# Kernel optimization log

Measured on AMD Instinct MI355X. Metric: run time of the kernel, lower is better.

Reference implementation:

```python
import jax, jax.numpy as jnp
import numpy as np

B, S, D, K = 8, 4096, 256, 8192
BETA = 0.25


def setup_inputs() -> dict:
    key = jax.random.key(0)
    k1, k2 = jax.random.split(key)
    return {
        "z": jax.random.normal(k1, (B, S, D), dtype=jnp.float32),
        "embed": jax.random.normal(k2, (K, D), dtype=jnp.float32),
    }


def reference(z, embed):
    # Inference-path VQ-EMA forward (EMA buffer updates are a no-grad side
    # effect only active in training mode; excluded from the pure reference).
    num_codes, dim = embed.shape
    z_flat = z.reshape(-1, dim)                      # [N, D]
    # squared-euclidean distances: ||z||^2 - 2 z.e^T + ||e||^2  -> [N, K]
    dist = ((z_flat * z_flat).sum(1, keepdims=True)
            - 2.0 * (z_flat @ embed.T)
            + (embed * embed).sum(1)[None, :])
    idx = jnp.argmin(dist, axis=1)                   # [N]
    z_q = embed[idx].reshape(z.shape)                # gather instead of onehot @ embed
    # commitment loss: beta * mse(stop_grad(z_q), z)
    loss = BETA * jnp.mean(jnp.square(jax.lax.stop_gradient(z_q) - z))
    # straight-through estimator
    z_q_st = z + jax.lax.stop_gradient(z_q - z)
    # perplexity from code usage histogram (scatter-add instead of onehot.mean)
    counts = jnp.zeros((num_codes,), dtype=z.dtype).at[idx].add(1.0)
    avg_probs = counts / idx.shape[0]
    perplexity = jnp.exp(-jnp.sum(avg_probs * jnp.log(avg_probs + 1e-12)))
    return z_q_st, loss, perplexity, idx.reshape(z.shape[:-1])
```

## Files before the change

kernel.cpp:

```cpp
#include <hip/hip_runtime.h>
#include <stdint.h>
#include <math.h>

#define NROWS 32768
#define DIM   256
#define KCODES 8192
#define BETA  0.25f
#define RSPLIT 64
#define NELEM 8388608
#define TAU 0.09375f

typedef float f32x4 __attribute__((ext_vector_type(4)));
typedef _Float16 v8h __attribute__((ext_vector_type(8)));
typedef unsigned short us4 __attribute__((ext_vector_type(4)));

__device__ inline unsigned int split1(float x) {
    _Float16 hf = (_Float16)x;
    _Float16 lf = (_Float16)(x - (float)hf);
    unsigned int h = __builtin_bit_cast(unsigned short, hf);
    unsigned int l = __builtin_bit_cast(unsigned short, lf);
    return h | (l << 16);
}

__device__ inline void gload_lds16(const void* g, void* l) {
    __builtin_amdgcn_global_load_lds(
        (const __attribute__((address_space(1))) void*)g,
        (__attribute__((address_space(3))) void*)l,
        16, 0, 0);
}

__device__ inline unsigned int fkey(float f) {
    unsigned int b = __float_as_uint(f);
    return (b & 0x80000000u) ? ~b : (b | 0x80000000u);
}

__global__ void prep_all(const float* __restrict__ z,
                         const float* __restrict__ e,
                         unsigned short* __restrict__ zhi,
                         unsigned short* __restrict__ zlo,
                         unsigned short* __restrict__ ehi,
                         unsigned short* __restrict__ elo,
                         float* __restrict__ enrm,
                         float* __restrict__ counts,
                         float* __restrict__ lossAcc,
                         int* __restrict__ flagcnt) {
    if (blockIdx.x < 8192) {
        int t = blockIdx.x * 256 + threadIdx.x;
        float4 v = reinterpret_cast<const float4*>(z)[t];
        unsigned int p0 = split1(v.x);
        unsigned int p1 = split1(v.y);
        unsigned int p2 = split1(v.z);
        unsigned int p3 = split1(v.w);
        us4 h, l;
        h[0] = (unsigned short)p0; l[0] = (unsigned short)(p0 >> 16);
        h[1] = (unsigned short)p1; l[1] = (unsigned short)(p1 >> 16);
        h[2] = (unsigned short)p2; l[2] = (unsigned short)(p2 >> 16);
        h[3] = (unsigned short)p3; l[3] = (unsigned short)(p3 >> 16);
        reinterpret_cast<us4*>(zhi)[t] = h;
        reinterpret_cast<us4*>(zlo)[t] = l;
    } else {
        int row = blockIdx.x - 8192;
        int d = threadIdx.x;
        float x = e[(size_t)row * DIM + d];
        unsigned int p = split1(x);
        ehi[(size_t)row * DIM + d] = (unsigned short)p;
        elo[(size_t)row * DIM + d] = (unsigned short)(p >> 16);
        float sq = x * x;
        #pragma unroll
        for (int off = 32; off; off >>= 1) sq += __shfl_down(sq, off);
        __shared__ float ps[4];
        if ((threadIdx.x & 63) == 0) ps[threadIdx.x >> 6] = sq;
        __syncthreads();
        if (threadIdx.x == 0) {
            enrm[row] = 0.5f * (ps[0] + ps[1] + ps[2] + ps[3]);
            counts[row] = 0.f;
            if (row == 0) { *lossAcc = 0.f; *flagcnt = 0; }
        }
    }
}

__launch_bounds__(256, 2)
__global__ void gemm_hi_fused(const unsigned short* __restrict__ zhi,
                              const unsigned short* __restrict__ ehi,
                              const float* __restrict__ enrm,
                              int* __restrict__ colidx,
                              float* __restrict__ out_idx,
                              int* __restrict__ flagcnt,
                              int* __restrict__ flaglist,
                              unsigned long long* __restrict__ rkey) {
    __shared__ __align__(16) unsigned short Bs[4][128 * 64];
    __shared__ float rvv[4][64];
    __shared__ float rv2s[4][64];
    __shared__ int   rcc[4][64];

    const int tid = threadIdx.x;
    const int w = tid >> 6, l = tid & 63;
    const int lx = l & 15, quad = l >> 4;
    const int arow_base = blockIdx.x * 64;
    const int fr = lx & 7;
    const int ecol = w * 32 + lx;
    const int st_g = ((l & 7) ^ (l >> 3)) * 8;
    const int srow = tid >> 3;

    v8h af[4][8];
    #pragma unroll
    for (int mi = 0; mi < 4; ++mi) {
        const unsigned short* ap =
            zhi + (size_t)(arow_base + mi * 16 + lx) * DIM + quad * 8;
        #pragma unroll
        for (int ks = 0; ks < 8; ++ks)
            af[mi][ks] = *(const v8h*)(ap + ks * 32);
    }

    float esn0 = enrm[ecol];
    float esn1 = enrm[ecol + 16];

#define STAGE(BUF, NT, BK) do {                                               \
        const unsigned short* _s = ehi + (size_t)(NT) * (128 * DIM)           \
            + (size_t)srow * DIM + (BK) * 64 + st_g;                          \
        gload_lds16(_s,                    &Bs[BUF][(w * 8) * 64]);           \
        gload_lds16(_s + (size_t)32 * DIM, &Bs[BUF][(32 + w * 8) * 64]);      \
        gload_lds16(_s + (size_t)64 * DIM, &Bs[BUF][(64 + w * 8) * 64]);      \
        gload_lds16(_s + (size_t)96 * DIM, &Bs[BUF][(96 + w * 8) * 64]);      \
} while (0)

#define FENCE do {                                                            \
        asm volatile("s_waitcnt vmcnt(8)" ::: "memory");                      \
        __builtin_amdgcn_s_barrier();                                         \
        asm volatile("" ::: "memory");                                        \
} while (0)

#define READF(BUF) do {                                                       \
        _Pragma("unroll") for (int kc = 0; kc < 2; ++kc) {                    \
            const int gsw = ((kc * 4 + quad) ^ fr) * 8;                       \
            bf[kc * 2 + 0] = *(const v8h*)&Bs[BUF][(ecol) * 64 + gsw];        \
            bf[kc * 2 + 1] = *(const v8h*)&Bs[BUF][(ecol + 16) * 64 + gsw];   \
        }                                                                     \
} while (0)

#define MFMAS(BK) do {                                                        \
        __builtin_amdgcn_s_setprio(1);                                        \
        _Pragma("unroll") for (int kc = 0; kc < 2; ++kc)                      \
            _Pragma("unroll") for (int mi = 0; mi < 4; ++mi)                  \
                _Pragma("unroll") for (int ni = 0; ni < 2; ++ni)              \
                    acc[mi][ni] = __builtin_amdgcn_mfma_f32_16x16x32_f16(     \
                        af[mi][(BK) * 2 + kc], bf[kc * 2 + ni],               \
                        acc[mi][ni], 0, 0, 0);                                \
        __builtin_amdgcn_s_setprio(0);                                        \
} while (0)

#define INITACC do {                                                          \
        _Pragma("unroll") for (int mi = 0; mi < 4; ++mi) {                    \
            acc[mi][0] = (f32x4){-esn0, -esn0, -esn0, -esn0};                 \
            acc[mi][1] = (f32x4){-esn1, -esn1, -esn1, -esn1};                 \
        }                                                                     \
} while (0)

#define ESLOAD(NT) do {                                                       \
        const int _b = (NT) * 128 + ecol;                                     \
        esn0 = enrm[_b]; esn1 = enrm[_b + 16];                                \
} while (0)

#define EPILOGUE(NTV) do {                                                    \
        _Pragma("unroll") for (int ni = 0; ni < 2; ++ni) {                    \
            const int col = (NTV) * 128 + ecol + ni * 16;                     \
            _Pragma("unroll") for (int mi = 0; mi < 4; ++mi)                  \
                _Pragma("unroll") for (int r = 0; r < 4; ++r) {               \
                    const int s = mi * 4 + r;                                 \
                    const float a = acc[mi][ni][r];                           \
                    const bool gt = a > runm[s];                              \
                    runm2[s] = __builtin_amdgcn_fmed3f(a, runm[s], runm2[s]); \
                    runc[s] = gt ? col : runc[s];                             \
                    runm[s] = fmaxf(runm[s], a);                              \
                }                                                             \
        }                                                                     \
} while (0)

    float runm[16], runm2[16];
    int runc[16];
    #pragma unroll
    for (int s = 0; s < 16; ++s) {
        runm[s] = -3.0e38f; runm2[s] = -3.0e38f; runc[s] = 0x7fffffff;
    }

    f32x4 acc[4][2];
    v8h bf[4];
    STAGE(0, 0, 0);
    STAGE(1, 0, 1);

    for (int nt = 0; nt < 64; ++nt) {
        const int ntn = (nt + 1) & 63;
        STAGE(2, nt, 2);  FENCE; INITACC; READF(0); MFMAS(0);
        STAGE(3, nt, 3);  FENCE; READF(1); MFMAS(1); ESLOAD(ntn);
        STAGE(0, ntn, 0); FENCE; READF(2); MFMAS(2);
        STAGE(1, ntn, 1); FENCE; READF(3); MFMAS(3);
        EPILOGUE(nt);
    }
#undef STAGE
#undef FENCE
#undef READF
#undef MFMAS
#undef INITACC
#undef ESLOAD
#undef EPILOGUE

    #pragma unroll
    for (int s = 0; s < 16; ++s) {
        float m1 = runm[s], m2 = runm2[s];
        int c1 = runc[s];
        #pragma unroll
        for (int m = 1; m < 16; m <<= 1) {
            float o1 = __shfl_xor(m1, m);
            int oc = __shfl_xor(c1, m);
            float o2 = __shfl_xor(m2, m);
            float mn = fminf(m1, o1);
            m2 = fmaxf(fmaxf(m2, o2), mn);
            bool take = (o1 > m1) || (o1 == m1 && oc < c1);
            m1 = take ? o1 : m1;
            c1 = take ? oc : c1;
        }
        if (lx == 0) {
            const int rl = (s >> 2) * 16 + quad * 4 + (s & 3);
            rvv[w][rl] = m1; rcc[w][rl] = c1; rv2s[w][rl] = m2;
        }
    }
    __syncthreads();
    if (tid < 64) {
        float m1 = rvv[0][tid], m2 = rv2s[0][tid];
        int c1 = rcc[0][tid];
        #pragma unroll
        for (int q = 1; q < 4; ++q) {
            float o1 = rvv[q][tid], o2 = rv2s[q][tid];
            int oc = rcc[q][tid];
            float mn = fminf(m1, o1);
            m2 = fmaxf(fmaxf(m2, o2), mn);
            bool take = (o1 > m1) || (o1 == m1 && oc < c1);
            m1 = take ? o1 : m1;
            c1 = take ? oc : c1;
        }
        const float v1 = -m1, v2 = -m2;
        const int row = arow_base + tid;
        out_idx[row] = (float)c1;
        if (v2 - v1 < TAU) {
            int slot = atomicAdd(flagcnt, 1);
            flaglist[slot] = row;
            rkey[slot] = ~0ull;
            colidx[row] = -(slot + 1);
        } else {
            colidx[row] = c1;
        }
    }
}

__launch_bounds__(256, 2)
__global__ void rescue_gemm(const unsigned short* __restrict__ zhi,
                            const unsigned short* __restrict__ zlo,
                            const unsigned short* __restrict__ ehi,
                            const unsigned short* __restrict__ elo,
                            const float* __restrict__ enrm,
                            const int* __restrict__ flagcnt,
                            const int* __restrict__ flaglist,
                            unsigned long long* __restrict__ rkey) {
    __shared__ __align__(16) unsigned short As[128 * 64];
    __shared__ __align__(16) unsigned short Bs[128 * 64];
    __shared__ float rv[2][128];
    __shared__ int   rc[2][128];

    const int count = *flagcnt;
    const int tid = threadIdx.x;
    const int w = tid >> 6, l = tid & 63;
    const int lx = l & 15, quad = l >> 4;
    const int wm = w >> 1, wn = w & 1;
    const int cs = blockIdx.y;
    const int cbase_cs = cs * (KCODES / RSPLIT);

    const int st_row8 = l >> 3;
    const int st_g = (((l & 7) ^ (l >> 3)) * 8);
    const int fr_lx7 = lx & 7;

    for (int tb = blockIdx.x * 128; tb < count; tb += 32 * 128) {
        int arowj[4];
        #pragma unroll
        for (int j = 0; j < 4; ++j) {
            int li = tb + w * 32 + j * 8 + st_row8;
            arowj[j] = (li < count) ? flaglist[li] : 0;
        }

        float runv[16];
        int runc[16];
        #pragma unroll
        for (int s = 0; s < 16; ++s) { runv[s] = 3.0e38f; runc[s] = 0x7fffffff; }

        for (int nt = 0; nt < (KCODES / RSPLIT) / 128; ++nt) {
            const int colbase = cbase_cs + nt * 128;
            f32x4 acc[4][4];
            #pragma unroll
            for (int mi = 0; mi < 4; ++mi)
                #pragma unroll
                for (int ni = 0; ni < 4; ++ni) {
                    f32x4 zz = {0.f, 0.f, 0.f, 0.f};
                    acc[mi][ni] = zz;
                }

            #pragma unroll
            for (int seg = 0; seg < 3; ++seg) {
                const unsigned short* za = (seg == 2) ? zlo : zhi;
                const unsigned short* eb = (seg == 1) ? elo : ehi;
                for (int bk = 0; bk < 4; ++bk) {
                    const int ao = bk * 64;
                    __syncthreads();
                    #pragma unroll
                    for (int j = 0; j < 4; ++j) {
                        const int r = w * 32 + j * 8 + st_row8;
                        gload_lds16(za + (size_t)arowj[j] * DIM + ao + st_g,
                                    &As[(w * 32 + j * 8) * 64]);
                        gload_lds16(eb + (size_t)(colbase + r) * DIM + ao + st_g,
                                    &Bs[(w * 32 + j * 8) * 64]);
                    }
                    __syncthreads();
                    #pragma unroll
                    for (int kc = 0; kc < 2; ++kc) {
                        const int gsw = ((kc * 4 + quad) ^ fr_lx7) * 8;
                        v8h af[4], bfr[4];
                        #pragma unroll
                        for (int mi = 0; mi < 4; ++mi)
                            af[mi] = *(const v8h*)&As[(wm * 64 + mi * 16 + lx) * 64 + gsw];
                        #pragma unroll
                        for (int ni = 0; ni < 4; ++ni)
                            bfr[ni] = *(const v8h*)&Bs[(wn * 64 + ni * 16 + lx) * 64 + gsw];
                        #pragma unroll
                        for (int mi = 0; mi < 4; ++mi)
                            #pragma unroll
                            for (int ni = 0; ni < 4; ++ni)
                                acc[mi][ni] = __builtin_amdgcn_mfma_f32_16x16x32_f16(
                                    af[mi], bfr[ni], acc[mi][ni], 0, 0, 0);
                    }
                }
            }

            #pragma unroll
            for (int ni = 0; ni < 4; ++ni) {
                const int col = colbase + wn * 64 + ni * 16 + lx;
                const float es = enrm[col];
                #pragma unroll
                for (int mi = 0; mi < 4; ++mi)
                    #pragma unroll
                    for (int r = 0; r < 4; ++r) {
                        float sv = es - acc[mi][ni][r];
                        const int s = mi * 4 + r;
                        if (sv < runv[s]) { runv[s] = sv; runc[s] = col; }
                    }
            }
        }

        #pragma unroll
        for (int s = 0; s < 16; ++s) {
            float v = runv[s]; int c = runc[s];
            #pragma unroll
            for (int m = 1; m < 16; m <<= 1) {
                float ov = __shfl_xor(v, m);
                int oc = __shfl_xor(c, m);
                if (ov < v || (ov == v && oc < c)) { v = ov; c = oc; }
            }
            if (lx == 0) {
                const int mi = s >> 2, r = s & 3;
                const int rl = wm * 64 + mi * 16 + quad * 4 + r;
                rv[wn][rl] = v; rc[wn][rl] = c;
            }
        }
        __syncthreads();
        if (tid < 128) {
            float v0 = rv[0][tid]; int c0 = rc[0][tid];
            float v1 = rv[1][tid]; int c1 = rc[1][tid];
            if (v1 < v0 || (v1 == v0 && c1 < c0)) { v0 = v1; c0 = c1; }
            const int li = tb + tid;
            if (li < count) {
                unsigned long long key =
                    ((unsigned long long)fkey(v0) << 32) | (unsigned int)c0;
                atomicMin(&rkey[li], key);
            }
        }
        __syncthreads();
    }
}

__global__ void fused_out(const int* __restrict__ colidx,
                          const unsigned long long* __restrict__ rkey,
                          const float* __restrict__ z,
                          const float* __restrict__ embed,
                          float* __restrict__ out_zq,
                          float* __restrict__ out_idx,
                          float* __restrict__ counts,
                          float* __restrict__ lossAcc) {
    __shared__ int cidx[16];
    const int tid = threadIdx.x;
    if (tid < 16) {
        const int row = blockIdx.x * 16 + tid;
        int c = colidx[row];
        if (c < 0) {
            c = (int)(unsigned int)(rkey[-c - 1] & 0x1FFFull);
            out_idx[row] = (float)c;
        }
        cidx[tid] = c;
        atomicAdd(&counts[c], 1.0f);
    }
    __syncthreads();
    const int d = tid;
    float ls = 0.f;
    #pragma unroll 4
    for (int i = 0; i < 16; ++i) {
        const int row = blockIdx.x * 16 + i;
        const int c = cidx[i];
        const float zv = z[(size_t)row * DIM + d];
        const float ev = embed[(size_t)c * DIM + d];
        const float diff = ev - zv;
        out_zq[(size_t)row * DIM + d] = zv + diff;
        ls += diff * diff;
    }
    #pragma unroll
    for (int off = 32; off; off >>= 1) ls += __shfl_down(ls, off);
    __shared__ float ps[4];
    if ((tid & 63) == 0) ps[tid >> 6] = ls;
    __syncthreads();
    if (tid == 0) atomicAdd(lossAcc, ps[0] + ps[1] + ps[2] + ps[3]);
}

__global__ void finalize(const float* __restrict__ counts,
                         const float* __restrict__ lossAcc,
                         float* __restrict__ out_loss,
                         float* __restrict__ out_perp) {
    float h = 0.f;
    for (int k = threadIdx.x; k < KCODES; k += 256) {
        float p = counts[k] * (1.0f / (float)NROWS);
        h += p * logf(p + 1e-12f);
    }
    #pragma unroll
    for (int off = 32; off; off >>= 1) h += __shfl_down(h, off);
    __shared__ float ps[4];
    if ((threadIdx.x & 63) == 0) ps[threadIdx.x >> 6] = h;
    __syncthreads();
    if (threadIdx.x == 0) {
        *out_perp = expf(-(ps[0] + ps[1] + ps[2] + ps[3]));
        *out_loss = BETA * lossAcc[0] / (float)NELEM;
    }
}

extern "C" void kernel_launch(void* const* d_in, const int* in_sizes, int n_in,
                              void* d_out, int out_size, void* d_ws, size_t ws_size,
                              hipStream_t stream) {
    const float* z = (const float*)d_in[0];
    const float* embed = (const float*)d_in[1];
    char* ws = (char*)d_ws;

    unsigned short* zhi = (unsigned short*)(ws + 0);
    unsigned short* zlo = (unsigned short*)(ws + 16777216);
    unsigned short* ehi = (unsigned short*)(ws + 33554432);
    unsigned short* elo = (unsigned short*)(ws + 37748736);
    float* enrm    = (float*)(ws + 41943040);
    int*   colidx  = (int*)  (ws + 43548672);
    float* counts  = (float*)(ws + 43679744);
    float* lossAcc = (float*)(ws + 43712512);
    int*   flagcnt = (int*)  (ws + 43712516);
    int*   flaglist = (int*) (ws + 43712520);
    unsigned long long* rkey = (unsigned long long*)(ws + 43843592);

    float* out = (float*)d_out;
    float* out_zq   = out;
    float* out_loss = out + 8388608;
    float* out_perp = out + 8388609;
    float* out_idx  = out + 8388610;

    prep_all<<<16384, 256, 0, stream>>>(z, embed, zhi, zlo, ehi, elo, enrm,
                                        counts, lossAcc, flagcnt);
    gemm_hi_fused<<<NROWS / 64, 256, 0, stream>>>(
        zhi, ehi, enrm, colidx, out_idx, flagcnt, flaglist, rkey);
    rescue_gemm<<<dim3(32, RSPLIT), 256, 0, stream>>>(
        zhi, zlo, ehi, elo, enrm, flagcnt, flaglist, rkey);
    fused_out<<<NROWS / 16, 256, 0, stream>>>(colidx, rkey, z, embed,
                                              out_zq, out_idx, counts, lossAcc);
    finalize<<<1, 256, 0, stream>>>(counts, lossAcc, out_loss, out_perp);
}
```

Baseline: 371.9 us.

## Restructure rescue GEMM to register-resident A rows and early-exit empty blocks

```diff
diff --git a/kernel.cpp b/kernel.cpp
--- a/kernel.cpp
+++ b/kernel.cpp
@@ -6,7 +6,6 @@
 #define DIM   256
 #define KCODES 8192
 #define BETA  0.25f
-#define RSPLIT 64
 #define NELEM 8388608
 #define TAU 0.09375f
 
@@ -261,96 +260,93 @@
                             const int* __restrict__ flagcnt,
                             const int* __restrict__ flaglist,
                             unsigned long long* __restrict__ rkey) {
-    __shared__ __align__(16) unsigned short As[128 * 64];
     __shared__ __align__(16) unsigned short Bs[128 * 64];
-    __shared__ float rv[2][128];
-    __shared__ int   rc[2][128];
+    __shared__ float rvv[4][64];
+    __shared__ int   rcc[4][64];
 
     const int count = *flagcnt;
+    if ((int)blockIdx.x * 64 >= count) return;
+    const int cbase = blockIdx.y * 256;
+
     const int tid = threadIdx.x;
     const int w = tid >> 6, l = tid & 63;
     const int lx = l & 15, quad = l >> 4;
-    const int wm = w >> 1, wn = w & 1;
-    const int cs = blockIdx.y;
-    const int cbase_cs = cs * (KCODES / RSPLIT);
-
-    const int st_row8 = l >> 3;
-    const int st_g = (((l & 7) ^ (l >> 3)) * 8);
-    const int fr_lx7 = lx & 7;
-
-    for (int tb = blockIdx.x * 128; tb < count; tb += 32 * 128) {
-        int arowj[4];
-        #pragma unroll
-        for (int j = 0; j < 4; ++j) {
-            int li = tb + w * 32 + j * 8 + st_row8;
-            arowj[j] = (li < count) ? flaglist[li] : 0;
-        }
-
-        float runv[16];
-        int runc[16];
-        #pragma unroll
-        for (int s = 0; s < 16; ++s) { runv[s] = 3.0e38f; runc[s] = 0x7fffffff; }
-
-        for (int nt = 0; nt < (KCODES / RSPLIT) / 128; ++nt) {
-            const int colbase = cbase_cs + nt * 128;
-            f32x4 acc[4][4];
-            #pragma unroll
-            for (int mi = 0; mi < 4; ++mi)
+    const int fr = lx & 7;
+    const int ecol = w * 32 + lx;
+    const int st_g = ((l & 7) ^ (l >> 3)) * 8;
+    const int srow = tid >> 3;
+
+    for (int tb = blockIdx.x * 64; tb < count; tb += 32 * 64) {
+        int arow[4];
+        #pragma unroll
+        for (int mi = 0; mi < 4; ++mi) {
+            const int li = tb + mi * 16 + lx;
+            arow[mi] = (li < count) ? flaglist[li] : 0;
+        }
+
+        f32x4 acc[4][4];
+        #pragma unroll
+        for (int mi = 0; mi < 4; ++mi)
+            #pragma unroll
+            for (int j = 0; j < 4; ++j)
+                acc[mi][j] = (f32x4){0.f, 0.f, 0.f, 0.f};
+
+        #pragma unroll
+        for (int seg = 0; seg < 3; ++seg) {
+            const unsigned short* za = (seg == 2) ? zlo : zhi;
+            const unsigned short* eb = (seg == 1) ? elo : ehi;
+            v8h af[4][8];
+            #pragma unroll
+            for (int mi = 0; mi < 4; ++mi) {
+                const unsigned short* ap = za + (size_t)arow[mi] * DIM + quad * 8;
                 #pragma unroll
-                for (int ni = 0; ni < 4; ++ni) {
-                    f32x4 zz = {0.f, 0.f, 0.f, 0.f};
-                    acc[mi][ni] = zz;
-                }
-
-            #pragma unroll
-            for (int seg = 0; seg < 3; ++seg) {
-                const unsigned short* za = (seg == 2) ? zlo : zhi;
-                const unsigned short* eb = (seg == 1) ? elo : ehi;
+                for (int ks = 0; ks < 8; ++ks)
+                    af[mi][ks] = *(const v8h*)(ap + ks * 32);
+            }
+            #pragma unroll
+            for (int nt = 0; nt < 2; ++nt) {
                 for (int bk = 0; bk < 4; ++bk) {
-                    const int ao = bk * 64;
                     __syncthreads();
-                    #pragma unroll
-                    for (int j = 0; j < 4; ++j) {
-                        const int r = w * 32 + j * 8 + st_row8;
-                        gload_lds16(za + (size_t)arowj[j] * DIM + ao + st_g,
-                                    &As[(w * 32 + j * 8) * 64]);
-                        gload_lds16(eb + (size_t)(colbase + r) * DIM + ao + st_g,
-                                    &Bs[(w * 32 + j * 8) * 64]);
-                    }
+                    const unsigned short* _s = eb
+                        + (size_t)(cbase + nt * 128 + srow) * DIM + bk * 64 + st_g;
+                    gload_lds16(_s,                    &Bs[(w * 8) * 64]);
+                    gload_lds16(_s + (size_t)32 * DIM, &Bs[(32 + w * 8) * 64]);
+                    gload_lds16(_s + (size_t)64 * DIM, &Bs[(64 + w * 8) * 64]);
+                    gload_lds16(_s + (size_t)96 * DIM, &Bs[(96 + w * 8) * 64]);
                     __syncthreads();
                     #pragma unroll
                     for (int kc = 0; kc < 2; ++kc) {
-                        const int gsw = ((kc * 4 + quad) ^ fr_lx7) * 8;
-                        v8h af[4], bfr[4];
+                        const int gsw = ((kc * 4 + quad) ^ fr) * 8;
+                        v8h b0 = *(const v8h*)&Bs[(ecol) * 64 + gsw];
+                        v8h b1 = *(const v8h*)&Bs[(ecol + 16) * 64 + gsw];
                         #pragma unroll
-                        for (int mi = 0; mi < 4; ++mi)
-                            af[mi] = *(const v8h*)&As[(wm * 64 + mi * 16 + lx) * 64 + gsw];
-                        #pragma unroll
-                        for (int ni = 0; ni < 4; ++ni)
-                            bfr[ni] = *(const v8h*)&Bs[(wn * 64 + ni * 16 + lx) * 64 + gsw];
-                        #pragma unroll
-                        for (int mi = 0; mi < 4; ++mi)
-                            #pragma unroll
-                            for (int ni = 0; ni < 4; ++ni)
-                                acc[mi][ni] = __builtin_amdgcn_mfma_f32_16x16x32_f16(
-                                    af[mi], bfr[ni], acc[mi][ni], 0, 0, 0);
+                        for (int mi = 0; mi < 4; ++mi) {
+                            acc[mi][nt * 2 + 0] = __builtin_amdgcn_mfma_f32_16x16x32_f16(
+                                af[mi][bk * 2 + kc], b0, acc[mi][nt * 2 + 0], 0, 0, 0);
+                            acc[mi][nt * 2 + 1] = __builtin_amdgcn_mfma_f32_16x16x32_f16(
+                                af[mi][bk * 2 + kc], b1, acc[mi][nt * 2 + 1], 0, 0, 0);
+                        }
                     }
                 }
             }
-
-            #pragma unroll
-            for (int ni = 0; ni < 4; ++ni) {
-                const int col = colbase + wn * 64 + ni * 16 + lx;
-                const float es = enrm[col];
+        }
+
+        float runv[16];
+        int runc[16];
+        #pragma unroll
+        for (int s = 0; s < 16; ++s) { runv[s] = 3.0e38f; runc[s] = 0x7fffffff; }
+        #pragma unroll
+        for (int j = 0; j < 4; ++j) {
+            const int col = cbase + (j >> 1) * 128 + ecol + (j & 1) * 16;
+            const float es = enrm[col];
+            #pragma unroll
+            for (int mi = 0; mi < 4; ++mi)
                 #pragma unroll
-                for (int mi = 0; mi < 4; ++mi)
-                    #pragma unroll
-                    for (int r = 0; r < 4; ++r) {
-                        float sv = es - acc[mi][ni][r];
-                        const int s = mi * 4 + r;
-                        if (sv < runv[s]) { runv[s] = sv; runc[s] = col; }
-                    }
-            }
+                for (int r = 0; r < 4; ++r) {
+                    const float sv = es - acc[mi][j][r];
+                    const int s = mi * 4 + r;
+                    if (sv < runv[s]) { runv[s] = sv; runc[s] = col; }
+                }
         }
 
         #pragma unroll
@@ -363,16 +359,18 @@
                 if (ov < v || (ov == v && oc < c)) { v = ov; c = oc; }
             }
             if (lx == 0) {
-                const int mi = s >> 2, r = s & 3;
-                const int rl = wm * 64 + mi * 16 + quad * 4 + r;
-                rv[wn][rl] = v; rc[wn][rl] = c;
+                const int rl = (s >> 2) * 16 + quad * 4 + (s & 3);
+                rvv[w][rl] = v; rcc[w][rl] = c;
             }
         }
         __syncthreads();
-        if (tid < 128) {
-            float v0 = rv[0][tid]; int c0 = rc[0][tid];
-            float v1 = rv[1][tid]; int c1 = rc[1][tid];
-            if (v1 < v0 || (v1 == v0 && c1 < c0)) { v0 = v1; c0 = c1; }
+        if (tid < 64) {
+            float v0 = rvv[0][tid]; int c0 = rcc[0][tid];
+            #pragma unroll
+            for (int q = 1; q < 4; ++q) {
+                float v1 = rvv[q][tid]; int c1 = rcc[q][tid];
+                if (v1 < v0 || (v1 == v0 && c1 < c0)) { v0 = v1; c0 = c1; }
+            }
             const int li = tb + tid;
             if (li < count) {
                 unsigned long long key =
@@ -474,7 +472,7 @@
                                         counts, lossAcc, flagcnt);
     gemm_hi_fused<<<NROWS / 64, 256, 0, stream>>>(
         zhi, ehi, enrm, colidx, out_idx, flagcnt, flaglist, rkey);
-    rescue_gemm<<<dim3(32, RSPLIT), 256, 0, stream>>>(
+    rescue_gemm<<<dim3(32, 32), 256, 0, stream>>>(
         zhi, zlo, ehi, elo, enrm, flagcnt, flaglist, rkey);
     fused_out<<<NROWS / 16, 256, 0, stream>>>(colidx, rkey, z, embed,
                                               out_zq, out_idx, counts, lossAcc);
```

After: 453.4 us. 1.22x slower.
